# Kernel tuning notes

Hardware: AMD Instinct MI355X
Metric: run time of the kernel (lower is better)

Reference implementation:

```python
import jax, jax.numpy as jnp
import numpy as np
import math

B, N, D_IN, D_OUT, H = 8, 1024, 512, 512, 8
DH = D_OUT // H  # 64
SCALE = math.sqrt(DH)

def setup_inputs() -> dict:
    key = jax.random.key(0)
    ks = jax.random.split(key, 10)
    s_in = 1.0 / math.sqrt(D_IN)
    s_out = 1.0 / math.sqrt(D_OUT)
    return {
        "x": jax.random.normal(ks[0], (B, N, D_IN), dtype=jnp.float32),
        "Wq": jax.random.uniform(ks[1], (D_IN, D_OUT), jnp.float32, -s_in, s_in),
        "bq": jnp.zeros((D_OUT,), jnp.float32),
        "Wk": jax.random.uniform(ks[2], (D_IN, D_OUT), jnp.float32, -s_in, s_in),
        "bk": jnp.zeros((D_OUT,), jnp.float32),
        "Wv": jax.random.uniform(ks[3], (D_IN, D_OUT), jnp.float32, -s_in, s_in),
        "bv": jnp.zeros((D_OUT,), jnp.float32),
        "Wo": jax.random.uniform(ks[4], (D_OUT, D_OUT), jnp.float32, -s_out, s_out),
        "bo": jnp.zeros((D_OUT,), jnp.float32),
        # external distance-based positional bias buffer (num_heads, N, N)
        "pos_bias": 0.01 * jax.random.normal(ks[5], (H, N, N), dtype=jnp.float32),
    }

def reference(x, Wq, bq, Wk, bk, Wv, bv, Wo, bo, pos_bias):
    Bx, Nx, _ = x.shape
    # QKV projections -> (B, H, N, DH)
    def split_heads(t):
        return t.reshape(Bx, Nx, H, DH).transpose(0, 2, 1, 3)
    q = split_heads(x @ Wq + bq)
    k = split_heads(x @ Wk + bk)
    v = split_heads(x @ Wv + bv)
    # scaled dot-product scores with additive positional bias
    scores = jnp.einsum('bhnd,bhmd->bhnm', q, k) / SCALE + pos_bias[None]
    attn = jax.nn.softmax(scores, axis=-1)  # dropout p=0 (eval)
    out = jnp.einsum('bhnm,bhmd->bhnd', attn, v)
    out = out.transpose(0, 2, 1, 3).reshape(Bx, Nx, D_OUT)  # concat heads
    return out @ Wo + bo
```

## Files before the change

kernel.cpp:

```cpp
#include <hip/hip_runtime.h>
#include <hip/hip_bf16.h>
#include <stdint.h>


typedef __attribute__((ext_vector_type(4))) float f32x4;
typedef __attribute__((ext_vector_type(8))) short s16x8;
typedef __attribute__((ext_vector_type(4))) unsigned short u16x4;

union FragAB { s16x8 v; u16x4 h[2]; };

#define LOG2E 1.44269504089f
#define QSCALE (0.125f * LOG2E)

__device__ __forceinline__ unsigned short f2b(float f) {
  unsigned u = __builtin_bit_cast(unsigned, f);
  u = (u + 0x7FFFu + ((u >> 16) & 1u)) >> 16;
  return (unsigned short)u;
}
__device__ __forceinline__ unsigned short f2b_fast(float f) {
  return __builtin_bit_cast(unsigned short, __float2bfloat16(f));
}

__global__ __launch_bounds__(256) void convx_k(const float* __restrict__ x,
                                               unsigned short* __restrict__ xb) {
  int idx = blockIdx.x * 256 + threadIdx.x;
  f32x4 v = ((const f32x4*)x)[idx];
  u16x4 o;
#pragma unroll
  for (int j = 0; j < 4; j++) o[j] = f2b(v[j]);
  ((u16x4*)xb)[idx] = o;
}

__global__ __launch_bounds__(256) void wtrans4_k(const float* __restrict__ W0,
                                                 const float* __restrict__ W1,
                                                 const float* __restrict__ W2,
                                                 const float* __restrict__ W3,
                                                 unsigned short* __restrict__ Wt) {
  const int widx = blockIdx.x >> 10;
  const float* W = widx == 0 ? W0 : widx == 1 ? W1 : widx == 2 ? W2 : W3;
  const int idx = (blockIdx.x & 1023) * 256 + threadIdx.x;
  const int j = idx >> 9, k = idx & 511;
  Wt[((size_t)widx << 18) + idx] = f2b(W[k * 512 + j]);
}

__global__ __launch_bounds__(256, 2) void gemm_qkv_k(const unsigned short* __restrict__ A,
                                                     const unsigned short* __restrict__ Bt,
                                                     const float* __restrict__ bq,
                                                     const float* __restrict__ bk,
                                                     const float* __restrict__ bv,
                                                     unsigned short* __restrict__ outp) {
  __shared__ unsigned short At[2][128][36];
  __shared__ unsigned short Bts[2][128][36];
  const int tid = threadIdx.x;
  const int lane = tid & 63;
  const int w = tid >> 6;
  const int wm = w >> 1, wn = w & 1;
  const int g = lane >> 4, c = lane & 15;
  const int bn0 = (blockIdx.x % 12) * 128;
  const int bm0 = (blockIdx.x / 12) * 128;
  const int srow = tid >> 1;
  const int scol = (tid & 1) * 16;

  f32x4 acc[4][4];
#pragma unroll
  for (int i = 0; i < 4; i++)
#pragma unroll
    for (int j = 0; j < 4; j++) acc[i][j] = f32x4{0.f, 0.f, 0.f, 0.f};

  u16x4 ra[4], rb[4];
  auto ld = [&](int kt) {
    const u16x4* pa = (const u16x4*)(A + (size_t)(bm0 + srow) * 512 + kt * 32 + scol);
    const u16x4* pb = (const u16x4*)(Bt + (size_t)(bn0 + srow) * 512 + kt * 32 + scol);
#pragma unroll
    for (int j = 0; j < 4; j++) { ra[j] = pa[j]; rb[j] = pb[j]; }
  };
  auto st = [&](int b) {
    u16x4* da = (u16x4*)&At[b][srow][scol];
    u16x4* db = (u16x4*)&Bts[b][srow][scol];
#pragma unroll
    for (int j = 0; j < 4; j++) { da[j] = ra[j]; db[j] = rb[j]; }
  };

  ld(0);
  st(0);
  __syncthreads();

  for (int kt = 0; kt < 16; ++kt) {
    const int cb = kt & 1;
    if (kt < 15) ld(kt + 1);

    FragAB af[4], bf[4];
#pragma unroll
    for (int mi = 0; mi < 4; mi++) {
      const u16x4* p = (const u16x4*)&At[cb][wm * 64 + mi * 16 + c][g * 8];
      af[mi].h[0] = p[0]; af[mi].h[1] = p[1];
    }
#pragma unroll
    for (int ni = 0; ni < 4; ni++) {
      const u16x4* p = (const u16x4*)&Bts[cb][wn * 64 + ni * 16 + c][g * 8];
      bf[ni].h[0] = p[0]; bf[ni].h[1] = p[1];
    }
    __builtin_amdgcn_s_setprio(1);
#pragma unroll
    for (int mi = 0; mi < 4; mi++)
#pragma unroll
      for (int ni = 0; ni < 4; ni++)
        acc[mi][ni] = __builtin_amdgcn_mfma_f32_16x16x32_bf16(af[mi].v, bf[ni].v,
                                                              acc[mi][ni], 0, 0, 0);
    __builtin_amdgcn_s_setprio(0);

    if (kt < 15) {
      st(cb ^ 1);
      __syncthreads();
    }
  }

  const int qkv = (bn0 + wn * 64) >> 9;
  const float* bp = qkv == 0 ? bq : (qkv == 1 ? bk : bv);
  const float scale = qkv == 0 ? QSCALE : 1.0f;
#pragma unroll
  for (int mi = 0; mi < 4; mi++) {
#pragma unroll
    for (int ni = 0; ni < 4; ni++) {
      const int col = bn0 + wn * 64 + ni * 16 + c;
      const int c9 = col & 511;
      const float bvv = bp[c9];
#pragma unroll
      for (int m = 0; m < 4; m++) {
        const int row = bm0 + wm * 64 + mi * 16 + g * 4 + m;
        const float v = (acc[mi][ni][m] + bvv) * scale;
        const int b = row >> 10, n = row & 1023;
        const int hh = c9 >> 6, d = col & 63;
        outp[((size_t)qkv << 22) + ((size_t)((b << 3) + hh) << 16) +
             ((size_t)n << 6) + d] = f2b(v);
      }
    }
  }
}

__global__ __launch_bounds__(256, 2) void gemm_o_k(const unsigned short* __restrict__ A,
                                                   const unsigned short* __restrict__ Bt,
                                                   const float* __restrict__ bias,
                                                   float* __restrict__ outp) {
  __shared__ unsigned short At[2][128][36];
  __shared__ unsigned short Bts[2][128][36];
  const int tid = threadIdx.x;
  const int lane = tid & 63;
  const int w = tid >> 6;
  const int wm = w >> 1, wn = w & 1;
  const int g = lane >> 4, c = lane & 15;
  const int bn0 = (blockIdx.x & 3) * 128;
  const int bm0 = (blockIdx.x >> 2) * 128;
  const int srow = tid >> 1;
  const int scol = (tid & 1) * 16;

  f32x4 acc[4][4];
#pragma unroll
  for (int i = 0; i < 4; i++)
#pragma unroll
    for (int j = 0; j < 4; j++) acc[i][j] = f32x4{0.f, 0.f, 0.f, 0.f};

  u16x4 ra[4], rb[4];
  auto ld = [&](int kt) {
    const u16x4* pa = (const u16x4*)(A + (size_t)(bm0 + srow) * 512 + kt * 32 + scol);
    const u16x4* pb = (const u16x4*)(Bt + (size_t)(bn0 + srow) * 512 + kt * 32 + scol);
#pragma unroll
    for (int j = 0; j < 4; j++) { ra[j] = pa[j]; rb[j] = pb[j]; }
  };
  auto st = [&](int b) {
    u16x4* da = (u16x4*)&At[b][srow][scol];
    u16x4* db = (u16x4*)&Bts[b][srow][scol];
#pragma unroll
    for (int j = 0; j < 4; j++) { da[j] = ra[j]; db[j] = rb[j]; }
  };

  ld(0);
  st(0);
  __syncthreads();

  for (int kt = 0; kt < 16; ++kt) {
    const int cb = kt & 1;
    if (kt < 15) ld(kt + 1);

    FragAB af[4], bf[4];
#pragma unroll
    for (int mi = 0; mi < 4; mi++) {
      const u16x4* p = (const u16x4*)&At[cb][wm * 64 + mi * 16 + c][g * 8];
      af[mi].h[0] = p[0]; af[mi].h[1] = p[1];
    }
#pragma unroll
    for (int ni = 0; ni < 4; ni++) {
      const u16x4* p = (const u16x4*)&Bts[cb][wn * 64 + ni * 16 + c][g * 8];
      bf[ni].h[0] = p[0]; bf[ni].h[1] = p[1];
    }
    __builtin_amdgcn_s_setprio(1);
#pragma unroll
    for (int mi = 0; mi < 4; mi++)
#pragma unroll
      for (int ni = 0; ni < 4; ni++)
        acc[mi][ni] = __builtin_amdgcn_mfma_f32_16x16x32_bf16(af[mi].v, bf[ni].v,
                                                              acc[mi][ni], 0, 0, 0);
    __builtin_amdgcn_s_setprio(0);

    if (kt < 15) {
      st(cb ^ 1);
      __syncthreads();
    }
  }

#pragma unroll
  for (int mi = 0; mi < 4; mi++) {
#pragma unroll
    for (int ni = 0; ni < 4; ni++) {
      const int col = bn0 + wn * 64 + ni * 16 + c;
      const float bv = bias[col];
#pragma unroll
      for (int m = 0; m < 4; m++) {
        const int row = bm0 + wm * 64 + mi * 16 + g * 4 + m;
        outp[(size_t)row * 512 + col] = acc[mi][ni][m] + bv;
      }
    }
  }
}

__global__ __launch_bounds__(512, 4) void attn_k(const unsigned short* __restrict__ Qb,
                                                 const unsigned short* __restrict__ Kb,
                                                 const unsigned short* __restrict__ Vb,
                                                 const float* __restrict__ pos_bias,
                                                 unsigned short* __restrict__ ao) {
  __shared__ unsigned short Klds[2][64][68];
  __shared__ unsigned short Vtlds[2][64][68];
  __shared__ unsigned short Plds[8][16][68];

  const int tid = threadIdx.x;
  const int lane = tid & 63;
  const int w = tid >> 6;
  const int g = lane >> 4, c = lane & 15;
  const int qt = blockIdx.x;
  const int bh = blockIdx.y;
  const int h = bh & 7;
  const size_t bhq = (size_t)bh << 16;
  const int q0 = qt * 128 + w * 16;

  FragAB aq[2];
#pragma unroll
  for (int kk = 0; kk < 2; kk++) {
    const u16x4* p =
        (const u16x4*)(Qb + bhq + ((size_t)(q0 + c) << 6) + kk * 32 + g * 8);
    aq[kk].h[0] = p[0]; aq[kk].h[1] = p[1];
  }

  f32x4 acco[4];
#pragma unroll
  for (int ni = 0; ni < 4; ni++) acco[ni] = f32x4{0.f, 0.f, 0.f, 0.f};
  float l_part[4] = {0.f, 0.f, 0.f, 0.f};

  const int krow = tid >> 4;
  const int kslot = (tid & 15) * 4;
  const int vd = tid & 63;
  const int vs = w;

  u16x4 kr[2], vr[2];
  auto stageLoad = [&](int k0) {
    kr[0] = *(const u16x4*)(Kb + bhq + ((size_t)(k0 + krow) << 6) + kslot);
    kr[1] = *(const u16x4*)(Kb + bhq + ((size_t)(k0 + krow + 32) << 6) + kslot);
    const unsigned short* pv = Vb + bhq + ((size_t)(k0 + vs * 8) << 6) + vd;
    union { unsigned short s[8]; u16x4 v[2]; } vv;
#pragma unroll
    for (int j = 0; j < 8; j++) vv.s[j] = pv[(size_t)j << 6];
    vr[0] = vv.v[0]; vr[1] = vv.v[1];
  };
  auto stageWrite = [&](int b) {
    *(u16x4*)&Klds[b][krow][kslot] = kr[0];
    *(u16x4*)&Klds[b][krow + 32][kslot] = kr[1];
    *(u16x4*)&Vtlds[b][vd][vs * 8] = vr[0];
    *(u16x4*)&Vtlds[b][vd][vs * 8 + 4] = vr[1];
  };

  const float* pbp =
      pos_bias + ((size_t)h << 20) + ((size_t)(q0 + g * 4) << 10) + c;

  stageLoad(0);
  stageWrite(0);
  __syncthreads();

  for (int kt = 0; kt < 16; ++kt) {
    const int buf = kt & 1;
    const int k0 = kt * 64;
    if (kt < 15) stageLoad(k0 + 64);

    float pb[16];
#pragma unroll
    for (int m = 0; m < 4; m++)
#pragma unroll
      for (int ni = 0; ni < 4; ni++)
        pb[m * 4 + ni] = pbp[((size_t)m << 10) + k0 + ni * 16] * LOG2E;

    FragAB bk[4][2];
#pragma unroll
    for (int ni = 0; ni < 4; ni++)
#pragma unroll
      for (int kk = 0; kk < 2; kk++) {
        const u16x4* p = (const u16x4*)&Klds[buf][ni * 16 + c][kk * 32 + g * 8];
        bk[ni][kk].h[0] = p[0]; bk[ni][kk].h[1] = p[1];
      }
    f32x4 accs[4];
    __builtin_amdgcn_s_setprio(1);
#pragma unroll
    for (int ni = 0; ni < 4; ni++) {
      f32x4 s = f32x4{0.f, 0.f, 0.f, 0.f};
      s = __builtin_amdgcn_mfma_f32_16x16x32_bf16(aq[0].v, bk[ni][0].v, s, 0, 0, 0);
      s = __builtin_amdgcn_mfma_f32_16x16x32_bf16(aq[1].v, bk[ni][1].v, s, 0, 0, 0);
      accs[ni] = s;
    }
    __builtin_amdgcn_s_setprio(0);

#pragma unroll
    for (int m = 0; m < 4; m++) {
      const float p0 = __builtin_amdgcn_exp2f(accs[0][m] + pb[m * 4 + 0]);
      const float p1 = __builtin_amdgcn_exp2f(accs[1][m] + pb[m * 4 + 1]);
      const float p2 = __builtin_amdgcn_exp2f(accs[2][m] + pb[m * 4 + 2]);
      const float p3 = __builtin_amdgcn_exp2f(accs[3][m] + pb[m * 4 + 3]);
      l_part[m] += (p0 + p1) + (p2 + p3);
      Plds[w][g * 4 + m][0 * 16 + c] = f2b_fast(p0);
      Plds[w][g * 4 + m][1 * 16 + c] = f2b_fast(p1);
      Plds[w][g * 4 + m][2 * 16 + c] = f2b_fast(p2);
      Plds[w][g * 4 + m][3 * 16 + c] = f2b_fast(p3);
    }

    asm volatile("s_waitcnt lgkmcnt(0)" ::: "memory");

    FragAB vb2[4][2], pa[2];
#pragma unroll
    for (int kc = 0; kc < 2; kc++) {
      const u16x4* p = (const u16x4*)&Plds[w][c][kc * 32 + g * 8];
      pa[kc].h[0] = p[0]; pa[kc].h[1] = p[1];
    }
#pragma unroll
    for (int ni = 0; ni < 4; ni++)
#pragma unroll
      for (int kc = 0; kc < 2; kc++) {
        const u16x4* p = (const u16x4*)&Vtlds[buf][ni * 16 + c][kc * 32 + g * 8];
        vb2[ni][kc].h[0] = p[0]; vb2[ni][kc].h[1] = p[1];
      }
    __builtin_amdgcn_s_setprio(1);
#pragma unroll
    for (int ni = 0; ni < 4; ni++) {
      acco[ni] = __builtin_amdgcn_mfma_f32_16x16x32_bf16(pa[0].v, vb2[ni][0].v,
                                                         acco[ni], 0, 0, 0);
      acco[ni] = __builtin_amdgcn_mfma_f32_16x16x32_bf16(pa[1].v, vb2[ni][1].v,
                                                         acco[ni], 0, 0, 0);
    }
    __builtin_amdgcn_s_setprio(0);

    if (kt < 15) {
      stageWrite(buf ^ 1);
      __syncthreads();
    }
  }

  const int b = bh >> 3;
  float inv[4];
#pragma unroll
  for (int m = 0; m < 4; m++) {
    float l = l_part[m];
    l += __shfl_xor(l, 1);
    l += __shfl_xor(l, 2);
    l += __shfl_xor(l, 4);
    l += __shfl_xor(l, 8);
    inv[m] = 1.f / l;
  }
#pragma unroll
  for (int ni = 0; ni < 4; ni++)
#pragma unroll
    for (int m = 0; m < 4; m++) {
      const int n = q0 + g * 4 + m;
      ao[((size_t)(b * 1024 + n) << 9) + h * 64 + ni * 16 + c] =
          f2b(acco[ni][m] * inv[m]);
    }
}

extern "C" void kernel_launch(void* const* d_in, const int* in_sizes, int n_in,
                              void* d_out, int out_size, void* d_ws, size_t ws_size,
                              hipStream_t stream) {
  (void)in_sizes; (void)n_in; (void)out_size; (void)ws_size;
  const float* x  = (const float*)d_in[0];
  const float* Wq = (const float*)d_in[1];
  const float* bq = (const float*)d_in[2];
  const float* Wk = (const float*)d_in[3];
  const float* bk = (const float*)d_in[4];
  const float* Wv = (const float*)d_in[5];
  const float* bv = (const float*)d_in[6];
  const float* Wo = (const float*)d_in[7];
  const float* bo = (const float*)d_in[8];
  const float* pbias = (const float*)d_in[9];

  char* p = (char*)d_ws;
  unsigned short* xb  = (unsigned short*)p; p += (size_t)8192 * 512 * 2;
  unsigned short* WT  = (unsigned short*)p; p += (size_t)4 * 512 * 512 * 2;
  unsigned short* Qb  = (unsigned short*)p; p += (size_t)3 * 64 * 1024 * 64 * 2;
  unsigned short* AO  = (unsigned short*)p;

  unsigned short* WoT = WT + (size_t)3 * 512 * 512;
  unsigned short* Kb  = Qb + (size_t)64 * 1024 * 64;
  unsigned short* Vb  = Kb + (size_t)64 * 1024 * 64;

  convx_k<<<4096, 256, 0, stream>>>(x, xb);
  wtrans4_k<<<4096, 256, 0, stream>>>(Wq, Wk, Wv, Wo, WT);
  gemm_qkv_k<<<768, 256, 0, stream>>>(xb, WT, bq, bk, bv, Qb);
  attn_k<<<dim3(8, 64), 512, 0, stream>>>(Qb, Kb, Vb, pbias, AO);
  gemm_o_k<<<256, 256, 0, stream>>>(AO, WoT, bo, (float*)d_out);
}
```

Before: 94.23 us.

## Transpose score MFMA for vectorized pos_bias loads; fuse prep kernels with tiled transpose

The attention kernel now computes the score tile transposed (K as the A operand), so each lane holds four consecutive key columns for one query row. This lets pos_bias be read as float4 vectors, prefetched one iteration ahead into double-buffered registers, and lets P be written to LDS as packed bf16 pairs. Row sums then need only two cross-lane shuffles. Separately, the x conversion and weight transpose kernels are merged into one launch, and the weight transpose goes through an LDS tile so that global reads and writes are coalesced. The cost is more registers for the prefetched bias and extra shuffles in the epilogue.

```diff
diff --git a/kernel.cpp b/kernel.cpp
--- a/kernel.cpp
+++ b/kernel.cpp
@@ -7,7 +7,7 @@
 typedef __attribute__((ext_vector_type(8))) short s16x8;
 typedef __attribute__((ext_vector_type(4))) unsigned short u16x4;
 
-union FragAB { s16x8 v; u16x4 h[2]; };
+union FragAB { s16x8 v; u16x4 h[2]; unsigned u[4]; };
 
 #define LOG2E 1.44269504089f
 #define QSCALE (0.125f * LOG2E)
@@ -17,30 +17,48 @@
   u = (u + 0x7FFFu + ((u >> 16) & 1u)) >> 16;
   return (unsigned short)u;
 }
-__device__ __forceinline__ unsigned short f2b_fast(float f) {
-  return __builtin_bit_cast(unsigned short, __float2bfloat16(f));
-}
-
-__global__ __launch_bounds__(256) void convx_k(const float* __restrict__ x,
-                                               unsigned short* __restrict__ xb) {
-  int idx = blockIdx.x * 256 + threadIdx.x;
-  f32x4 v = ((const f32x4*)x)[idx];
-  u16x4 o;
-#pragma unroll
-  for (int j = 0; j < 4; j++) o[j] = f2b(v[j]);
-  ((u16x4*)xb)[idx] = o;
-}
-
-__global__ __launch_bounds__(256) void wtrans4_k(const float* __restrict__ W0,
-                                                 const float* __restrict__ W1,
-                                                 const float* __restrict__ W2,
-                                                 const float* __restrict__ W3,
-                                                 unsigned short* __restrict__ Wt) {
-  const int widx = blockIdx.x >> 10;
+__device__ __forceinline__ unsigned pack2(float lo, float hi) {
+  return ((unsigned)f2b(hi) << 16) | (unsigned)f2b(lo);
+}
+
+__global__ __launch_bounds__(256) void prep_k(const float* __restrict__ x,
+                                              unsigned short* __restrict__ xb,
+                                              const float* __restrict__ W0,
+                                              const float* __restrict__ W1,
+                                              const float* __restrict__ W2,
+                                              const float* __restrict__ W3,
+                                              unsigned short* __restrict__ Wt) {
+  __shared__ float ld[64][68];
+  const int t = threadIdx.x;
+  if (blockIdx.x < 4096) {
+    int idx = blockIdx.x * 256 + t;
+    f32x4 v = ((const f32x4*)x)[idx];
+    u16x4 o;
+#pragma unroll
+    for (int j = 0; j < 4; j++) o[j] = f2b(v[j]);
+    ((u16x4*)xb)[idx] = o;
+    return;
+  }
+  const int bid2 = blockIdx.x - 4096;
+  const int widx = bid2 >> 6;
+  const int tile = bid2 & 63;
+  const int trow = tile >> 3, tcol = tile & 7;
   const float* W = widx == 0 ? W0 : widx == 1 ? W1 : widx == 2 ? W2 : W3;
-  const int idx = (blockIdx.x & 1023) * 256 + threadIdx.x;
-  const int j = idx >> 9, k = idx & 511;
-  Wt[((size_t)widx << 18) + idx] = f2b(W[k * 512 + j]);
+  const int r = t >> 2, cc = (t & 3) * 16;
+  const float* src = W + (size_t)(trow * 64 + r) * 512 + tcol * 64 + cc;
+#pragma unroll
+  for (int u = 0; u < 4; u++)
+    ((f32x4*)&ld[r][cc])[u] = ((const f32x4*)src)[u];
+  __syncthreads();
+  unsigned short* dst = Wt + ((size_t)widx << 18) + (size_t)(tcol * 64 + r) * 512 +
+                        trow * 64 + cc;
+#pragma unroll
+  for (int u = 0; u < 4; u++) {
+    u16x4 o;
+#pragma unroll
+    for (int e = 0; e < 4; e++) o[e] = f2b(ld[cc + u * 4 + e][r]);
+    ((u16x4*)dst)[u] = o;
+  }
 }
 
 __global__ __launch_bounds__(256, 2) void gemm_qkv_k(const unsigned short* __restrict__ A,
@@ -81,8 +99,7 @@
     for (int j = 0; j < 4; j++) { da[j] = ra[j]; db[j] = rb[j]; }
   };
 
-  ld(0);
-  st(0);
+  ld(0); st(0);
   __syncthreads();
 
   for (int kt = 0; kt < 16; ++kt) {
@@ -174,8 +191,7 @@
     for (int j = 0; j < 4; j++) { da[j] = ra[j]; db[j] = rb[j]; }
   };
 
-  ld(0);
-  st(0);
+  ld(0); st(0);
   __syncthreads();
 
   for (int kt = 0; kt < 16; ++kt) {
@@ -252,8 +268,8 @@
 
   f32x4 acco[4];
 #pragma unroll
-  for (int ni = 0; ni < 4; ni++) acco[ni] = f32x4{0.f, 0.f, 0.f, 0.f};
-  float l_part[4] = {0.f, 0.f, 0.f, 0.f};
+  for (int nd = 0; nd < 4; nd++) acco[nd] = f32x4{0.f, 0.f, 0.f, 0.f};
+  float lsum = 0.f;
 
   const int krow = tid >> 4;
   const int kslot = (tid & 15) * 4;
@@ -261,10 +277,10 @@
   const int vs = w;
 
   u16x4 kr[2], vr[2];
-  auto stageLoad = [&](int k0) {
-    kr[0] = *(const u16x4*)(Kb + bhq + ((size_t)(k0 + krow) << 6) + kslot);
-    kr[1] = *(const u16x4*)(Kb + bhq + ((size_t)(k0 + krow + 32) << 6) + kslot);
-    const unsigned short* pv = Vb + bhq + ((size_t)(k0 + vs * 8) << 6) + vd;
+  auto stageLoad = [&](int k0n) {
+    kr[0] = *(const u16x4*)(Kb + bhq + ((size_t)(k0n + krow) << 6) + kslot);
+    kr[1] = *(const u16x4*)(Kb + bhq + ((size_t)(k0n + krow + 32) << 6) + kslot);
+    const unsigned short* pv = Vb + bhq + ((size_t)(k0n + vs * 8) << 6) + vd;
     union { unsigned short s[8]; u16x4 v[2]; } vv;
 #pragma unroll
     for (int j = 0; j < 8; j++) vv.s[j] = pv[(size_t)j << 6];
@@ -277,24 +293,25 @@
     *(u16x4*)&Vtlds[b][vd][vs * 8 + 4] = vr[1];
   };
 
-  const float* pbp =
-      pos_bias + ((size_t)h << 20) + ((size_t)(q0 + g * 4) << 10) + c;
+  const float* pbB = pos_bias + ((size_t)h << 20) + ((size_t)(q0 + c) << 10) + 4 * g;
 
   stageLoad(0);
   stageWrite(0);
   __syncthreads();
 
-  for (int kt = 0; kt < 16; ++kt) {
+  f32x4 pbX[4], pbY[4];
+#pragma unroll
+  for (int ni = 0; ni < 4; ni++) pbX[ni] = *(const f32x4*)(pbB + 16 * ni);
+
+  auto body = [&](int kt, f32x4 (&pbu)[4], f32x4 (&pbn)[4]) {
     const int buf = kt & 1;
     const int k0 = kt * 64;
-    if (kt < 15) stageLoad(k0 + 64);
-
-    float pb[16];
-#pragma unroll
-    for (int m = 0; m < 4; m++)
+    if (kt < 15) {
+      stageLoad(k0 + 64);
 #pragma unroll
       for (int ni = 0; ni < 4; ni++)
-        pb[m * 4 + ni] = pbp[((size_t)m << 10) + k0 + ni * 16] * LOG2E;
+        pbn[ni] = *(const f32x4*)(pbB + k0 + 64 + 16 * ni);
+    }
 
     FragAB bk[4][2];
 #pragma unroll
@@ -304,52 +321,50 @@
         const u16x4* p = (const u16x4*)&Klds[buf][ni * 16 + c][kk * 32 + g * 8];
         bk[ni][kk].h[0] = p[0]; bk[ni][kk].h[1] = p[1];
       }
-    f32x4 accs[4];
+    f32x4 sT[4];
     __builtin_amdgcn_s_setprio(1);
 #pragma unroll
     for (int ni = 0; ni < 4; ni++) {
       f32x4 s = f32x4{0.f, 0.f, 0.f, 0.f};
-      s = __builtin_amdgcn_mfma_f32_16x16x32_bf16(aq[0].v, bk[ni][0].v, s, 0, 0, 0);
-      s = __builtin_amdgcn_mfma_f32_16x16x32_bf16(aq[1].v, bk[ni][1].v, s, 0, 0, 0);
-      accs[ni] = s;
+      s = __builtin_amdgcn_mfma_f32_16x16x32_bf16(bk[ni][0].v, aq[0].v, s, 0, 0, 0);
+      s = __builtin_amdgcn_mfma_f32_16x16x32_bf16(bk[ni][1].v, aq[1].v, s, 0, 0, 0);
+      sT[ni] = s;
     }
     __builtin_amdgcn_s_setprio(0);
 
 #pragma unroll
-    for (int m = 0; m < 4; m++) {
-      const float p0 = __builtin_amdgcn_exp2f(accs[0][m] + pb[m * 4 + 0]);
-      const float p1 = __builtin_amdgcn_exp2f(accs[1][m] + pb[m * 4 + 1]);
-      const float p2 = __builtin_amdgcn_exp2f(accs[2][m] + pb[m * 4 + 2]);
-      const float p3 = __builtin_amdgcn_exp2f(accs[3][m] + pb[m * 4 + 3]);
-      l_part[m] += (p0 + p1) + (p2 + p3);
-      Plds[w][g * 4 + m][0 * 16 + c] = f2b_fast(p0);
-      Plds[w][g * 4 + m][1 * 16 + c] = f2b_fast(p1);
-      Plds[w][g * 4 + m][2 * 16 + c] = f2b_fast(p2);
-      Plds[w][g * 4 + m][3 * 16 + c] = f2b_fast(p3);
+    for (int ni = 0; ni < 4; ni++) {
+      const float p0 = __builtin_amdgcn_exp2f(fmaf(pbu[ni][0], LOG2E, sT[ni][0]));
+      const float p1 = __builtin_amdgcn_exp2f(fmaf(pbu[ni][1], LOG2E, sT[ni][1]));
+      const float p2 = __builtin_amdgcn_exp2f(fmaf(pbu[ni][2], LOG2E, sT[ni][2]));
+      const float p3 = __builtin_amdgcn_exp2f(fmaf(pbu[ni][3], LOG2E, sT[ni][3]));
+      lsum += (p0 + p1) + (p2 + p3);
+      *(unsigned*)&Plds[w][c][16 * ni + 4 * g]     = pack2(p0, p1);
+      *(unsigned*)&Plds[w][c][16 * ni + 4 * g + 2] = pack2(p2, p3);
     }
 
     asm volatile("s_waitcnt lgkmcnt(0)" ::: "memory");
 
-    FragAB vb2[4][2], pa[2];
+    FragAB paf[2], vb2[4][2];
 #pragma unroll
     for (int kc = 0; kc < 2; kc++) {
       const u16x4* p = (const u16x4*)&Plds[w][c][kc * 32 + g * 8];
-      pa[kc].h[0] = p[0]; pa[kc].h[1] = p[1];
-    }
-#pragma unroll
-    for (int ni = 0; ni < 4; ni++)
+      paf[kc].h[0] = p[0]; paf[kc].h[1] = p[1];
+    }
+#pragma unroll
+    for (int nd = 0; nd < 4; nd++)
 #pragma unroll
       for (int kc = 0; kc < 2; kc++) {
-        const u16x4* p = (const u16x4*)&Vtlds[buf][ni * 16 + c][kc * 32 + g * 8];
-        vb2[ni][kc].h[0] = p[0]; vb2[ni][kc].h[1] = p[1];
+        const u16x4* p = (const u16x4*)&Vtlds[buf][nd * 16 + c][kc * 32 + g * 8];
+        vb2[nd][kc].h[0] = p[0]; vb2[nd][kc].h[1] = p[1];
       }
     __builtin_amdgcn_s_setprio(1);
 #pragma unroll
-    for (int ni = 0; ni < 4; ni++) {
-      acco[ni] = __builtin_amdgcn_mfma_f32_16x16x32_bf16(pa[0].v, vb2[ni][0].v,
-                                                         acco[ni], 0, 0, 0);
-      acco[ni] = __builtin_amdgcn_mfma_f32_16x16x32_bf16(pa[1].v, vb2[ni][1].v,
-                                                         acco[ni], 0, 0, 0);
+    for (int nd = 0; nd < 4; nd++) {
+      acco[nd] = __builtin_amdgcn_mfma_f32_16x16x32_bf16(paf[0].v, vb2[nd][0].v,
+                                                         acco[nd], 0, 0, 0);
+      acco[nd] = __builtin_amdgcn_mfma_f32_16x16x32_bf16(paf[1].v, vb2[nd][1].v,
+                                                         acco[nd], 0, 0, 0);
     }
     __builtin_amdgcn_s_setprio(0);
 
@@ -357,27 +372,28 @@
       stageWrite(buf ^ 1);
       __syncthreads();
     }
-  }
-
+  };
+
+  for (int kt2 = 0; kt2 < 16; kt2 += 2) {
+    body(kt2, pbX, pbY);
+    body(kt2 + 1, pbY, pbX);
+  }
+
+  float l = lsum;
+  l += __shfl_xor(l, 16);
+  l += __shfl_xor(l, 32);
+  const float inv_c = 1.f / l;
   const int b = bh >> 3;
-  float inv[4];
 #pragma unroll
   for (int m = 0; m < 4; m++) {
-    float l = l_part[m];
-    l += __shfl_xor(l, 1);
-    l += __shfl_xor(l, 2);
-    l += __shfl_xor(l, 4);
-    l += __shfl_xor(l, 8);
-    inv[m] = 1.f / l;
-  }
-#pragma unroll
-  for (int ni = 0; ni < 4; ni++)
-#pragma unroll
-    for (int m = 0; m < 4; m++) {
-      const int n = q0 + g * 4 + m;
-      ao[((size_t)(b * 1024 + n) << 9) + h * 64 + ni * 16 + c] =
-          f2b(acco[ni][m] * inv[m]);
-    }
+    const float invm = __shfl(inv_c, g * 4 + m);
+    const int n = q0 + g * 4 + m;
+#pragma unroll
+    for (int nd = 0; nd < 4; nd++) {
+      ao[((size_t)(b * 1024 + n) << 9) + h * 64 + nd * 16 + c] =
+          f2b(acco[nd][m] * invm);
+    }
+  }
 }
 
 extern "C" void kernel_launch(void* const* d_in, const int* in_sizes, int n_in,
@@ -405,8 +421,7 @@
   unsigned short* Kb  = Qb + (size_t)64 * 1024 * 64;
   unsigned short* Vb  = Kb + (size_t)64 * 1024 * 64;
 
-  convx_k<<<4096, 256, 0, stream>>>(x, xb);
-  wtrans4_k<<<4096, 256, 0, stream>>>(Wq, Wk, Wv, Wo, WT);
+  prep_k<<<4352, 256, 0, stream>>>(x, xb, Wq, Wk, Wv, Wo, WT);
   gemm_qkv_k<<<768, 256, 0, stream>>>(xb, WT, bq, bk, bv, Qb);
   attn_k<<<dim3(8, 64), 512, 0, stream>>>(Qb, Kb, Vb, pbias, AO);
   gemm_o_k<<<256, 256, 0, stream>>>(AO, WoT, bo, (float*)d_out);
```

New measurement: 120.1 us. 1.27x slower.
